# Kernel optimization log

Hardware: AMD Instinct MI355X
Metric: run time of the kernel (lower is better)

The kernel has to match this reference:

```python
import jax, jax.numpy as jnp
import numpy as np

N = 50000      # nodes
E = 800000     # edges (avg degree 16)
F_IN = 128
H = 128        # hidden_channels
C = 10         # num_classes
S = 5          # Chebyshev order K
B = 8          # graphs in batch


def setup_inputs() -> dict:
    key = jax.random.key(0)
    ks = jax.random.split(key, 9)
    x = jax.random.normal(ks[0], (N, F_IN), jnp.float32)
    edge_index = jax.random.randint(ks[1], (2, E), 0, N, dtype=jnp.int64)
    batch = jnp.sort(jax.random.randint(ks[2], (N,), 0, B, dtype=jnp.int64))
    lambda_max = 2.0 * jnp.ones((B,), jnp.float32)
    W1 = jax.random.normal(ks[3], (S, F_IN, H), jnp.float32) * 0.05
    b1 = jax.random.normal(ks[4], (H,), jnp.float32) * 0.05
    W2 = jax.random.normal(ks[5], (S, H, H), jnp.float32) * 0.05
    b2 = jax.random.normal(ks[6], (H,), jnp.float32) * 0.05
    Wlin = jax.random.normal(ks[7], (H, C), jnp.float32) * 0.05
    blin = jax.random.normal(ks[8], (C,), jnp.float32) * 0.05
    return {"x": x, "edge_index": edge_index, "batch": batch,
            "lambda_max": lambda_max, "W1": W1, "b1": b1,
            "W2": W2, "b2": b2, "Wlin": Wlin, "blin": blin}


def _cheb_conv(x, row, col, w_edge, diag, W, b):
    # scaled Laplacian matvec: L_hat v = scatter(w_edge * v[col] -> row) + diag * v
    def Lhat(v):
        msg = v[col] * w_edge[:, None]                       # [E, d]
        return jax.ops.segment_sum(msg, row, num_segments=N) + diag[:, None] * v

    Tx0 = x
    out = Tx0 @ W[0]
    Tx1 = Lhat(Tx0)
    out = out + Tx1 @ W[1]
    for k in range(2, W.shape[0]):                           # Chebyshev recurrence
        Tx2 = 2.0 * Lhat(Tx1) - Tx0
        out = out + Tx2 @ W[k]
        Tx0, Tx1 = Tx1, Tx2
    return out + b


def reference(x, edge_index, batch, lambda_max, W1, b1, W2, b2, Wlin, blin):
    row, col = edge_index[0], edge_index[1]
    # sym-normalized Laplacian L = I - D^{-1/2} A D^{-1/2}; L_hat = 2L/lambda_max - I
    deg = jax.ops.segment_sum(jnp.ones((E,), x.dtype), row, num_segments=N)
    dis = jnp.where(deg > 0, jax.lax.rsqrt(jnp.maximum(deg, 1e-12)), 0.0)
    lam_e = lambda_max[batch[row]]                           # per-edge lambda_max
    w_edge = -2.0 * dis[row] * dis[col] / lam_e              # off-diagonal of L_hat
    diag = 2.0 / lambda_max[batch] - 1.0                     # diagonal of L_hat per node

    h = jax.nn.relu(_cheb_conv(x, row, col, w_edge, diag, W1, b1))
    h = jax.nn.relu(_cheb_conv(h, row, col, w_edge, diag, W2, b2))

    # global_mean_pool over batch assignment
    sums = jax.ops.segment_sum(h, batch, num_segments=B)     # [B, H]
    counts = jax.ops.segment_sum(jnp.ones((N, 1), h.dtype), batch, num_segments=B)
    pooled = sums / jnp.maximum(counts, 1.0)
    return pooled @ Wlin + blin                              # [B, C] logits (softmax unused in forward)
```

## Files before the change

kernel.cpp:

```cpp
#include <hip/hip_runtime.h>
#include <stdint.h>

typedef __attribute__((ext_vector_type(8))) short bf16x8;
typedef __attribute__((ext_vector_type(4))) float f32x4;

__device__ __forceinline__ float bf16lo_to_f(uint32_t u) { return __uint_as_float(u << 16); }
__device__ __forceinline__ float bf16hi_to_f(uint32_t u) { return __uint_as_float(u & 0xffff0000u); }
__device__ __forceinline__ uint16_t f_to_bf16(float f) {
    uint32_t u = __float_as_uint(f);
    uint32_t r = u + 0x7fff + ((u >> 16) & 1);
    return (uint16_t)(r >> 16);
}


#define BINCH 4096

__global__ void __launch_bounds__(256) k_bhist(const int* __restrict__ row,
                                               int* __restrict__ bhist, int E) {
    __shared__ int sh[256];
    int t = threadIdx.x;
    sh[t] = 0;
    __syncthreads();
    int stride = gridDim.x * blockDim.x;
    for (int e = blockIdx.x * blockDim.x + t; e < E; e += stride)
        atomicAdd(&sh[row[e] >> 8], 1);
    __syncthreads();
    if (sh[t]) atomicAdd(&bhist[t], sh[t]);
}

__global__ void k_bscan(const int* __restrict__ bhist, int* __restrict__ gbase,
                        int* __restrict__ gcur, float* __restrict__ mS, int nbk, int N) {
    __shared__ int sh[256];
    int t = threadIdx.x;
    int v = t < nbk ? bhist[t] : 0;
    sh[t] = v;
    __syncthreads();
    for (int o = 1; o < 256; o <<= 1) {
        int u = (t >= o) ? sh[t - o] : 0;
        __syncthreads();
        sh[t] += u;
        __syncthreads();
    }
    gbase[t] = sh[t] - v;
    gcur[t] = sh[t] - v;
    if (t == 255) gbase[256] = sh[255];
    if (t < 5) mS[(size_t)t * (N + 1) + N] = 0.f;
}

__global__ void __launch_bounds__(256) k_bin(const int* __restrict__ row,
        const int* __restrict__ col, int* __restrict__ gcur,
        uint32_t* __restrict__ bout, int E) {
    __shared__ uint32_t stage[BINCH];
    __shared__ int hist[256], hscan[256], hcur[256], gofs[256];
    int t = threadIdx.x;
    int e0 = blockIdx.x * BINCH;
    int ecnt = min(BINCH, E - e0);
    hist[t] = 0;
    __syncthreads();
    for (int i = t; i < ecnt; i += 256)
        atomicAdd(&hist[row[e0 + i] >> 8], 1);
    __syncthreads();
    int v = hist[t];
    hscan[t] = v;
    __syncthreads();
    for (int o = 1; o < 256; o <<= 1) {
        int u = (t >= o) ? hscan[t - o] : 0;
        __syncthreads();
        hscan[t] += u;
        __syncthreads();
    }
    hcur[t] = hscan[t] - v;
    __syncthreads();
    for (int i = t; i < ecnt; i += 256) {
        int r = row[e0 + i];
        int p = atomicAdd(&hcur[r >> 8], 1);
        stage[p] = (uint32_t)(r & 255) | ((uint32_t)col[e0 + i] << 8);
    }
    __syncthreads();
    if (v > 0) gofs[t] = atomicAdd(&gcur[t], v);
    __syncthreads();
    for (int i = t; i < ecnt; i += 256) {
        int lo = 0, hi = 255;
        while (lo < hi) { int mid = (lo + hi) >> 1; if (hscan[mid] > i) hi = mid; else lo = mid + 1; }
        int b = lo;
        int local = i - (hscan[b] - hist[b]);
        bout[gofs[b] + local] = stage[i];
    }
}

__global__ void __launch_bounds__(256) k_deg2(const uint32_t* __restrict__ bout,
        const int* __restrict__ gbase, int* __restrict__ deg,
        int* __restrict__ psum, int N) {
    __shared__ int cnt[256];
    __shared__ int red[256];
    int t = threadIdx.x, b = blockIdx.x;
    cnt[t] = 0;
    __syncthreads();
    int s = gbase[b], epos = gbase[b + 1];
    for (int i = s + t; i < epos; i += 256)
        atomicAdd(&cnt[bout[i] & 255], 1);
    __syncthreads();
    int n = b * 256 + t;
    int d = cnt[t];
    if (n < N) deg[n] = d;
    red[t] = (n < N) ? ((d + 7) & ~7) : 0;
    __syncthreads();
    for (int o = 128; o > 0; o >>= 1) {
        if (t < o) red[t] += red[t + o];
        __syncthreads();
    }
    if (t == 0) psum[b] = red[0];
}

__global__ void k_offs(const int* __restrict__ deg, const int* __restrict__ psum,
                       int* __restrict__ offs,
                       const int* __restrict__ batch, const float* __restrict__ lam,
                       float* __restrict__ dis, float* __restrict__ diag,
                       int N, int nb) {
    __shared__ int pre[256];
    __shared__ int sh[256];
    int t = threadIdx.x, b = blockIdx.x;
    pre[t] = (t < b) ? psum[t] : 0;
    __syncthreads();
    for (int o = 128; o > 0; o >>= 1) {
        if (t < o) pre[t] += pre[t + o];
        __syncthreads();
    }
    int base = pre[0];
    __syncthreads();
    int idx = b * 256 + t;
    int d = idx < N ? deg[idx] : 0;
    int v = (d + 7) & ~7;
    sh[t] = v;
    __syncthreads();
    for (int o = 1; o < 256; o <<= 1) {
        int u = (t >= o) ? sh[t - o] : 0;
        __syncthreads();
        sh[t] += u;
        __syncthreads();
    }
    if (idx < N) {
        offs[idx] = base + sh[t] - v;
        dis[idx] = d > 0 ? rsqrtf((float)d) : 0.f;
        diag[idx] = 2.f / lam[batch[idx]] - 1.f;
    }
    if (b == nb - 1 && t == 255) offs[N] = base + sh[255];
}

__global__ void __launch_bounds__(256) k_ew(const uint32_t* __restrict__ bout,
        const int* __restrict__ gbase, const int* __restrict__ offs,
        const float* __restrict__ dis, const float* __restrict__ diag,
        uint2* __restrict__ ew, int N) {
    __shared__ int cur[256];
    __shared__ float srw[256];
    int t = threadIdx.x, b = blockIdx.x;
    int n = b * 256 + t;
    int o0 = n < N ? offs[n] : 0;
    cur[t] = o0;
    srw[t] = (n < N) ? (-dis[n] * (diag[n] + 1.0f)) : 0.f;
    __syncthreads();
    int s = gbase[b], epos = gbase[b + 1];
    for (int i = s + t; i < epos; i += 256) {
        uint32_t v = bout[i];
        int r = (int)(v & 255u);
        int c = (int)(v >> 8);
        int p = atomicAdd(&cur[r], 1);
        float w = srw[r] * dis[c];
        ew[p] = make_uint2((uint32_t)c << 7, __float_as_uint(w));
    }
    __syncthreads();
    if (n < N) {
        int e = cur[t];
        int pe = o0 + ((e - o0 + 7) & ~7);
        uint2 pad = make_uint2((uint32_t)N << 7, 0u);
        for (int p = e; p < pe; p++) ew[p] = pad;
    }
}

__global__ void k_prepw(const float* __restrict__ W1, uint16_t* __restrict__ Wt1,
                        const float* __restrict__ W2, uint16_t* __restrict__ Wt2) {
    int i = blockIdx.x * blockDim.x + threadIdx.x;
    const float* W = W1; uint16_t* Wt = Wt1;
    if (i >= 128 * 640) { i -= 128 * 640; W = W2; Wt = Wt2; }
    int o = i / 640, kk = i % 640;
    Wt[(size_t)o * 640 + kk] = f_to_bf16(W[(size_t)kk * 128 + o]);
}

__global__ void __launch_bounds__(256) k_castx(const float* __restrict__ x,
        uint16_t* __restrict__ Txb, int8_t* __restrict__ Txq,
        float* __restrict__ mS, int N) {
    int n = (blockIdx.x * blockDim.x + threadIdx.x) >> 6;
    int lane = threadIdx.x & 63;
    if (n >= N) return;
    float2 v = ((const float2*)x)[(size_t)n * 64 + lane];
    uint32_t p = (uint32_t)f_to_bf16(v.x) | ((uint32_t)f_to_bf16(v.y) << 16);
    ((uint32_t*)Txb)[(size_t)n * 64 + lane] = p;
    float m = fmaxf(fabsf(v.x), fabsf(v.y));
    for (int o = 1; o < 64; o <<= 1) m = fmaxf(m, __shfl_xor(m, o));
    float inv = m > 0.f ? 127.f / m : 0.f;
    int qx = (int)rintf(v.x * inv), qy = (int)rintf(v.y * inv);
    *(uint16_t*)(Txq + (size_t)n * 128 + 2 * lane) = (uint16_t)((qx & 0xff) | ((qy & 0xff) << 8));
    if (lane == 0) mS[n] = m > 0.f ? m * (1.f / 127.f) : 0.f;
}

__global__ void __launch_bounds__(256) k_lhat(
        int8_t* __restrict__ Txq, uint16_t* __restrict__ Txb,
        float* __restrict__ mS,
        const int* __restrict__ offs, const uint2* __restrict__ ew,
        const float* __restrict__ diag, int N,
        int src, int dst, int prev, float alpha, int use_prev) {
    int n = (blockIdx.x * blockDim.x + threadIdx.x) >> 6;
    int lane = threadIdx.x & 63;
    if (n >= N) return;
    int beg = offs[n], end = offs[n + 1];
    int h = lane >> 5, g = lane & 31;
    size_t sq = (size_t)(N + 1) * 128;
    const int8_t* srcq = Txq + (size_t)src * sq;
    const float* msrc = mS + (size_t)src * (N + 1);
    uint32_t lo4 = (uint32_t)g * 4;
    const uint2* ewh = ew + h;
    float a0 = 0.f, a1 = 0.f, a2 = 0.f, a3 = 0.f;
    if (beg < end) {
        uint2 ep[4];
#pragma unroll
        for (int p = 0; p < 4; p++) ep[p] = ewh[beg + 2 * p];
        int e = beg;
        while (true) {
            uint32_t q[4]; float mm[4], wv[4];
#pragma unroll
            for (int p = 0; p < 4; p++) {
                uint32_t co = ep[p].x;
                wv[p] = __uint_as_float(ep[p].y);
                q[p] = *(const uint32_t*)(srcq + co + lo4);
                mm[p] = *(const float*)((const char*)msrc + (co >> 5));
            }
            int e2 = e + 8;
            bool more = e2 < end;
            uint2 epn[4];
            if (more) {
#pragma unroll
                for (int p = 0; p < 4; p++) epn[p] = ewh[e2 + 2 * p];
            }
#pragma unroll
            for (int p = 0; p < 4; p++) {
                float f = wv[p] * mm[p];
                a0 = fmaf(f, (float)(int)(int8_t)(q[p] & 0xff), a0);
                a1 = fmaf(f, (float)(int)(int8_t)((q[p] >> 8) & 0xff), a1);
                a2 = fmaf(f, (float)(int)(int8_t)((q[p] >> 16) & 0xff), a2);
                a3 = fmaf(f, (float)(int)(int8_t)(q[p] >> 24), a3);
            }
            if (!more) break;
            e = e2;
#pragma unroll
            for (int p = 0; p < 4; p++) ep[p] = epn[p];
        }
    }
    a0 += __shfl_xor(a0, 32);
    a1 += __shfl_xor(a1, 32);
    a2 += __shfl_xor(a2, 32);
    a3 += __shfl_xor(a3, 32);
    uint32_t rq = (uint32_t)n * 128 + lo4;
    uint32_t qs = *(const uint32_t*)(srcq + rq);
    float ssc = msrc[n] * diag[n];
    a0 = fmaf(ssc, (float)(int)(int8_t)(qs & 0xff), a0);
    a1 = fmaf(ssc, (float)(int)(int8_t)((qs >> 8) & 0xff), a1);
    a2 = fmaf(ssc, (float)(int)(int8_t)((qs >> 16) & 0xff), a2);
    a3 = fmaf(ssc, (float)(int)(int8_t)(qs >> 24), a3);
    float f0 = alpha * a0, f1 = alpha * a1, f2 = alpha * a2, f3 = alpha * a3;
    if (use_prev) {
        uint32_t qp = *(const uint32_t*)(Txq + (size_t)prev * sq + rq);
        float sp = mS[(size_t)prev * (N + 1) + n];
        f0 = fmaf(-sp, (float)(int)(int8_t)(qp & 0xff), f0);
        f1 = fmaf(-sp, (float)(int)(int8_t)((qp >> 8) & 0xff), f1);
        f2 = fmaf(-sp, (float)(int)(int8_t)((qp >> 16) & 0xff), f2);
        f3 = fmaf(-sp, (float)(int)(int8_t)(qp >> 24), f3);
    }
    if (h == 0) {
        uint2 pk;
        pk.x = (uint32_t)f_to_bf16(f0) | ((uint32_t)f_to_bf16(f1) << 16);
        pk.y = (uint32_t)f_to_bf16(f2) | ((uint32_t)f_to_bf16(f3) << 16);
        *(uint2*)(Txb + (size_t)dst * (size_t)(N + 1) * 128 + (size_t)n * 128 + g * 4) = pk;
    }
    float m = fmaxf(fmaxf(fabsf(f0), fabsf(f1)), fmaxf(fabsf(f2), fabsf(f3)));
#pragma unroll
    for (int o = 1; o < 32; o <<= 1) m = fmaxf(m, __shfl_xor(m, o));
    float inv = m > 0.f ? 127.f / m : 0.f;
    if (h == 0) {
        int q0 = (int)rintf(f0 * inv), q1 = (int)rintf(f1 * inv);
        int q2 = (int)rintf(f2 * inv), q3 = (int)rintf(f3 * inv);
        uint32_t pkq = (uint32_t)(q0 & 0xff) | ((uint32_t)(q1 & 0xff) << 8) |
                       ((uint32_t)(q2 & 0xff) << 16) | ((uint32_t)(q3 & 0xff) << 24);
        *(uint32_t*)(Txq + (size_t)dst * sq + rq) = pkq;
    }
    if (lane == 0) mS[(size_t)dst * (N + 1) + n] = m * (1.f / 127.f);
}

#define BM 128
#define BK 64
#define LDT 72
#define LDC 132

__global__ void __launch_bounds__(256) k_gemm(
        const uint16_t* __restrict__ A, size_t sstride,
        const uint16_t* __restrict__ Bt,
        const float* __restrict__ bias,
        uint16_t* __restrict__ out2b,
        int8_t* __restrict__ out2q,
        float* __restrict__ msOut,
        float* __restrict__ pooled,
        const int* __restrict__ batch,
        int M, int Kdim) {
    __shared__ uint16_t smem[BM * LDT + 128 * LDT];
    uint16_t* As = smem;
    uint16_t* Bs = smem + BM * LDT;
    uint16_t* Ct = smem;
    int t = threadIdx.x;
    int w = t >> 6, lane = t & 63;
    int row0 = blockIdx.x * BM;
    int mrow = (w >> 1) * 64, ncol = (w & 1) * 64;

    int ar[4], akc[4];
#pragma unroll
    for (int rep = 0; rep < 4; rep++) {
        int d = rep * 256 + t;
        ar[rep] = d >> 3; akc[rep] = d & 7;
    }

    f32x4 acc[4][4];
#pragma unroll
    for (int i = 0; i < 4; i++)
#pragma unroll
        for (int j = 0; j < 4; j++) acc[i][j] = (f32x4){0.f, 0.f, 0.f, 0.f};

    bf16x8 pa[4], pb[4];
#pragma unroll
    for (int rep = 0; rep < 4; rep++) {
        int grow = row0 + ar[rep];
        int kk = akc[rep] * 8;
        bf16x8 va = {0, 0, 0, 0, 0, 0, 0, 0};
        if (grow < M)
            va = *(const bf16x8*)(A + (size_t)(kk >> 7) * sstride + (size_t)grow * 128 + (kk & 127));
        pa[rep] = va;
        pb[rep] = *(const bf16x8*)(Bt + (size_t)ar[rep] * Kdim + kk);
    }

    for (int k0 = 0; k0 < Kdim; k0 += BK) {
#pragma unroll
        for (int rep = 0; rep < 4; rep++) {
            *(bf16x8*)(&As[ar[rep] * LDT + akc[rep] * 8]) = pa[rep];
            *(bf16x8*)(&Bs[ar[rep] * LDT + akc[rep] * 8]) = pb[rep];
        }
        __syncthreads();
        int kn = k0 + BK;
        if (kn < Kdim) {
#pragma unroll
            for (int rep = 0; rep < 4; rep++) {
                int grow = row0 + ar[rep];
                int kk = kn + akc[rep] * 8;
                bf16x8 va = {0, 0, 0, 0, 0, 0, 0, 0};
                if (grow < M)
                    va = *(const bf16x8*)(A + (size_t)(kk >> 7) * sstride + (size_t)grow * 128 + (kk & 127));
                pa[rep] = va;
                pb[rep] = *(const bf16x8*)(Bt + (size_t)ar[rep] * Kdim + kk);
            }
        }
#pragma unroll
        for (int ks = 0; ks < BK; ks += 32) {
            bf16x8 af[4], bfr[4];
#pragma unroll
            for (int i = 0; i < 4; i++) {
                int r = mrow + i * 16 + (lane & 15);
                af[i] = *(const bf16x8*)(&As[r * LDT + ks + (lane >> 4) * 8]);
            }
#pragma unroll
            for (int j = 0; j < 4; j++) {
                int c = ncol + j * 16 + (lane & 15);
                bfr[j] = *(const bf16x8*)(&Bs[c * LDT + ks + (lane >> 4) * 8]);
            }
#pragma unroll
            for (int i = 0; i < 4; i++)
#pragma unroll
                for (int j = 0; j < 4; j++)
                    acc[i][j] = __builtin_amdgcn_mfma_f32_16x16x32_bf16(af[i], bfr[j], acc[i][j], 0, 0, 0);
        }
        __syncthreads();
    }

#pragma unroll
    for (int j = 0; j < 4; j++) {
        int c = ncol + j * 16 + (lane & 15);
        float bv = bias[c];
#pragma unroll
        for (int i = 0; i < 4; i++) {
            int rloc = mrow + i * 16 + (lane >> 4) * 4;
#pragma unroll
            for (int r = 0; r < 4; r++) {
                float v = acc[i][j][r] + bv;
                v = v > 0.f ? v : 0.f;
                Ct[(rloc + r) * LDC + c] = f_to_bf16(v);
            }
        }
    }
    __syncthreads();

    if (out2b) {
#pragma unroll
        for (int rep = 0; rep < 8; rep++) {
            int d = rep * 256 + t;
            int r = d >> 4, c8 = (d & 15) * 8;
            int grow = row0 + r;
            if (grow < M) {
                bf16x8 v = *(const bf16x8*)(&Ct[r * LDC + c8]);
                *(bf16x8*)(out2b + (size_t)grow * 128 + c8) = v;
            }
        }
    }
    if (out2q) {
        int r = t >> 1, half = t & 1;
        int grow = row0 + r;
        float vmax = 0.f;
        for (int j = 0; j < 32; j++) {
            uint32_t u = *(const uint32_t*)(&Ct[r * LDC + half * 64 + j * 2]);
            vmax = fmaxf(vmax, fmaxf(fabsf(bf16lo_to_f(u)), fabsf(bf16hi_to_f(u))));
        }
        vmax = fmaxf(vmax, __shfl_xor(vmax, 1));
        if (grow < M) {
            float inv = vmax > 0.f ? 127.f / vmax : 0.f;
            for (int j0 = 0; j0 < 16; j0++) {
                uint32_t u0 = *(const uint32_t*)(&Ct[r * LDC + half * 64 + j0 * 4]);
                uint32_t u1 = *(const uint32_t*)(&Ct[r * LDC + half * 64 + j0 * 4 + 2]);
                int q0 = (int)rintf(bf16lo_to_f(u0) * inv);
                int q1 = (int)rintf(bf16hi_to_f(u0) * inv);
                int q2 = (int)rintf(bf16lo_to_f(u1) * inv);
                int q3 = (int)rintf(bf16hi_to_f(u1) * inv);
                uint32_t pk = (uint32_t)(q0 & 0xff) | ((uint32_t)(q1 & 0xff) << 8) |
                              ((uint32_t)(q2 & 0xff) << 16) | ((uint32_t)(q3 & 0xff) << 24);
                *(uint32_t*)(out2q + (size_t)grow * 128 + half * 64 + j0 * 4) = pk;
            }
            if (half == 0) msOut[grow] = vmax * (1.f / 127.f);
        }
    }
    if (pooled) {
        int f = t & 127, r0 = (t >> 7) * 64;
        float accp = 0.f;
        int curb = -1;
        for (int r = r0; r < r0 + 64; ++r) {
            int grow = row0 + r;
            if (grow >= M) break;
            int b = batch[grow];
            if (b != curb) {
                if (curb >= 0) atomicAdd(&pooled[curb * 128 + f], accp);
                accp = 0.f; curb = b;
            }
            accp += __uint_as_float(((uint32_t)Ct[r * LDC + f]) << 16);
        }
        if (curb >= 0) atomicAdd(&pooled[curb * 128 + f], accp);
    }
}

__global__ void k_final(const float* __restrict__ pooled, const int* __restrict__ batch,
                        const float* __restrict__ Wlin, const float* __restrict__ blin,
                        float* __restrict__ out, int N, int B_, int C_) {
    __shared__ int cnt[64];
    int t = threadIdx.x;
    if (t < B_) {
        auto lb = [&](int v) {
            int lo = 0, hi = N;
            while (lo < hi) {
                int mid = (lo + hi) >> 1;
                if (batch[mid] < v) lo = mid + 1; else hi = mid;
            }
            return lo;
        };
        cnt[t] = lb(t + 1) - lb(t);
    }
    __syncthreads();
    if (t < B_ * C_) {
        int b = t / C_, c = t % C_;
        float inv = 1.f / fmaxf((float)cnt[b], 1.f);
        float acc = blin[c];
        for (int f = 0; f < 128; ++f) acc += pooled[b * 128 + f] * inv * Wlin[f * C_ + c];
        out[t] = acc;
    }
}

extern "C" void kernel_launch(void* const* d_in, const int* in_sizes, int n_in,
                              void* d_out, int out_size, void* d_ws, size_t ws_size,
                              hipStream_t stream) {
    const float* x    = (const float*)d_in[0];
    const int*   edge = (const int*)d_in[1];
    const int*   batch= (const int*)d_in[2];
    const float* lam  = (const float*)d_in[3];
    const float* W1   = (const float*)d_in[4];
    const float* b1   = (const float*)d_in[5];
    const float* W2   = (const float*)d_in[6];
    const float* b2   = (const float*)d_in[7];
    const float* Wlin = (const float*)d_in[8];
    const float* blin = (const float*)d_in[9];
    const int E  = in_sizes[1] / 2;
    const int N  = in_sizes[2];
    const int B_ = in_sizes[3];
    const int* row = edge;
    const int* col = edge + E;

    char* ws = (char*)d_ws;
    size_t off = 0;
    auto take = [&](size_t bytes) -> char* {
        char* p = ws + off;
        off = (off + bytes + 255) & ~(size_t)255;
        return p;
    };
    uint16_t* Txb    = (uint16_t*)take((size_t)5 * (N + 1) * 128 * 2);
    int8_t*   Txq    = (int8_t*)take((size_t)5 * (N + 1) * 128);
    uint2*    ew     = (uint2*)take(((size_t)E + 8 * (size_t)N) * 8);
    float*    mS     = (float*)take((size_t)5 * (N + 1) * 4);
    int*      deg    = (int*)take((size_t)N * 4);
    int*      offs   = (int*)take((size_t)(N + 1) * 4);
    float*    dis    = (float*)take((size_t)N * 4);
    float*    diag   = (float*)take((size_t)N * 4);
    uint16_t* Wt1    = (uint16_t*)take((size_t)128 * 640 * 2);
    uint16_t* Wt2    = (uint16_t*)take((size_t)128 * 640 * 2);
    float*    pooled = (float*)take((size_t)B_ * 128 * 4);
    int*      bhist  = (int*)take(257 * 4);
    int*      gbase  = (int*)take(257 * 4);
    int*      gcur   = (int*)take(257 * 4);
    const int nb = (N + 255) / 256;
    int*      psum   = (int*)take((size_t)nb * 4);
    uint32_t* bout   = (uint32_t*)((char*)Txb + (size_t)4 * (N + 1) * 256);

    hipMemsetAsync(pooled, 0, (size_t)B_ * 128 * 4 + 257 * 4, stream);

    k_bhist<<<112, 256, 0, stream>>>(row, bhist, E);
    k_bscan<<<1, 256, 0, stream>>>(bhist, gbase, gcur, mS, nb, N);
    k_bin<<<(E + BINCH - 1) / BINCH, 256, 0, stream>>>(row, col, gcur, bout, E);
    k_deg2<<<nb, 256, 0, stream>>>(bout, gbase, deg, psum, N);
    k_offs<<<nb, 256, 0, stream>>>(deg, psum, offs, batch, lam, dis, diag, N, nb);
    k_ew<<<nb, 256, 0, stream>>>(bout, gbase, offs, dis, diag, ew, N);
    k_prepw<<<(2 * 128 * 640) / 256, 256, 0, stream>>>(W1, Wt1, W2, Wt2);
    k_castx<<<(N + 3) / 4, 256, 0, stream>>>(x, Txb, Txq, mS, N);

    const int lblocks = (N + 3) / 4;
    const int gblocks = (N + BM - 1) / BM;
    const size_t ss = (size_t)(N + 1) * 128;

    k_lhat<<<lblocks, 256, 0, stream>>>(Txq, Txb, mS, offs, ew, diag, N, 0, 1, 0, 1.f, 0);
    k_lhat<<<lblocks, 256, 0, stream>>>(Txq, Txb, mS, offs, ew, diag, N, 1, 2, 0, 2.f, 1);
    k_lhat<<<lblocks, 256, 0, stream>>>(Txq, Txb, mS, offs, ew, diag, N, 2, 3, 1, 2.f, 1);
    k_lhat<<<lblocks, 256, 0, stream>>>(Txq, Txb, mS, offs, ew, diag, N, 3, 4, 2, 2.f, 1);
    k_gemm<<<gblocks, 256, 0, stream>>>(Txb, ss, Wt1, b1,
                                        Txb , Txq , mS ,
                                        (float*)nullptr, batch, N, 640);

    k_lhat<<<lblocks, 256, 0, stream>>>(Txq, Txb, mS, offs, ew, diag, N, 0, 1, 0, 1.f, 0);
    k_lhat<<<lblocks, 256, 0, stream>>>(Txq, Txb, mS, offs, ew, diag, N, 1, 2, 0, 2.f, 1);
    k_lhat<<<lblocks, 256, 0, stream>>>(Txq, Txb, mS, offs, ew, diag, N, 2, 3, 1, 2.f, 1);
    k_lhat<<<lblocks, 256, 0, stream>>>(Txq, Txb, mS, offs, ew, diag, N, 3, 4, 2, 2.f, 1);
    k_gemm<<<gblocks, 256, 0, stream>>>(Txb, ss, Wt2, b2,
                                        (uint16_t*)nullptr, (int8_t*)nullptr, (float*)nullptr,
                                        pooled, batch, N, 640);

    k_final<<<1, 128, 0, stream>>>(pooled, batch, Wlin, blin, (float*)d_out, N, B_, 10);
}
```

Measured before the change: 469.3 us.

## Merge preprocessing and Chebyshev recurrence launches into cooperative persistent kernels

Replaces the eight preprocessing kernels with one cooperative kernel that runs the phases separated by grid.sync(). It also replaces the four per-layer L_hat launches with one persistent cooperative kernel that loops over nodes and prefetches the next node's offsets. The goal is to cut kernel launch overhead and tail idle time between the many short dependent launches. In exchange, the persistent grid is capped by occupancy, which may lower parallelism for latency hiding in the gather phase. The old multi-launch path remains as a fallback if the cooperative launch fails.

```diff
diff --git a/kernel.cpp b/kernel.cpp
--- a/kernel.cpp
+++ b/kernel.cpp
@@ -1,5 +1,8 @@
 #include <hip/hip_runtime.h>
+#include <hip/hip_cooperative_groups.h>
 #include <stdint.h>
+
+namespace cg = cooperative_groups;
 
 typedef __attribute__((ext_vector_type(8))) short bf16x8;
 typedef __attribute__((ext_vector_type(4))) float f32x4;
@@ -203,16 +206,203 @@
     if (lane == 0) mS[n] = m > 0.f ? m * (1.f / 127.f) : 0.f;
 }
 
-__global__ void __launch_bounds__(256) k_lhat(
+__global__ void __launch_bounds__(256) k_pre(
+        const float* __restrict__ x,
+        const int* __restrict__ row, const int* __restrict__ col,
+        const int* __restrict__ batch, const float* __restrict__ lam,
+        const float* __restrict__ W1, uint16_t* __restrict__ Wt1,
+        const float* __restrict__ W2, uint16_t* __restrict__ Wt2,
+        int* __restrict__ bhist, int* __restrict__ gbase, int* __restrict__ gcur,
+        uint32_t* __restrict__ bout, int* __restrict__ deg, int* __restrict__ psum,
+        int* __restrict__ offs, float* __restrict__ dis, float* __restrict__ diag,
+        uint2* __restrict__ ew, float* __restrict__ mS,
+        uint16_t* __restrict__ Txb, int8_t* __restrict__ Txq,
+        int E, int N, int nb, int nchunks) {
+    __shared__ uint32_t shb[5120];
+    cg::grid_group grid = cg::this_grid();
+    int t = threadIdx.x, b = blockIdx.x;
+    int gstride = gridDim.x * 256;
+
+    {
+        int* sh = (int*)shb;
+        sh[t] = 0;
+        __syncthreads();
+        for (int e = b * 256 + t; e < E; e += gstride)
+            atomicAdd(&sh[row[e] >> 8], 1);
+        __syncthreads();
+        if (sh[t]) atomicAdd(&bhist[t], sh[t]);
+    }
+    for (int i = b * 256 + t; i < 2 * 128 * 640; i += gstride) {
+        int ii = i;
+        const float* W = W1; uint16_t* Wt = Wt1;
+        if (ii >= 128 * 640) { ii -= 128 * 640; W = W2; Wt = Wt2; }
+        int o = ii / 640, kk = ii % 640;
+        Wt[(size_t)o * 640 + kk] = f_to_bf16(W[(size_t)kk * 128 + o]);
+    }
+    {
+        int lane = t & 63;
+        int gw = b * 4 + (t >> 6);
+        int tw = gridDim.x * 4;
+        for (int n = gw; n < N; n += tw) {
+            float2 v = ((const float2*)x)[(size_t)n * 64 + lane];
+            uint32_t p = (uint32_t)f_to_bf16(v.x) | ((uint32_t)f_to_bf16(v.y) << 16);
+            ((uint32_t*)Txb)[(size_t)n * 64 + lane] = p;
+            float m = fmaxf(fabsf(v.x), fabsf(v.y));
+            for (int o = 1; o < 64; o <<= 1) m = fmaxf(m, __shfl_xor(m, o));
+            float inv = m > 0.f ? 127.f / m : 0.f;
+            int qx = (int)rintf(v.x * inv), qy = (int)rintf(v.y * inv);
+            *(uint16_t*)(Txq + (size_t)n * 128 + 2 * lane) =
+                (uint16_t)((qx & 0xff) | ((qy & 0xff) << 8));
+            if (lane == 0) mS[n] = m > 0.f ? m * (1.f / 127.f) : 0.f;
+        }
+    }
+    grid.sync();
+
+    if (b == 0) {
+        int* sh = (int*)shb;
+        int v = bhist[t];
+        sh[t] = v;
+        __syncthreads();
+        for (int o = 1; o < 256; o <<= 1) {
+            int u = (t >= o) ? sh[t - o] : 0;
+            __syncthreads();
+            sh[t] += u;
+            __syncthreads();
+        }
+        gbase[t] = sh[t] - v;
+        gcur[t] = sh[t] - v;
+        if (t == 255) gbase[256] = sh[255];
+        if (t < 5) mS[(size_t)t * (N + 1) + N] = 0.f;
+    }
+    grid.sync();
+
+    if (b < nchunks) {
+        uint32_t* stage = shb;
+        int* hist  = (int*)(shb + 4096);
+        int* hscan = (int*)(shb + 4352);
+        int* hcur  = (int*)(shb + 4608);
+        int* gofs  = (int*)(shb + 4864);
+        int e0 = b * BINCH;
+        int ecnt = min(BINCH, E - e0);
+        hist[t] = 0;
+        __syncthreads();
+        for (int i = t; i < ecnt; i += 256)
+            atomicAdd(&hist[row[e0 + i] >> 8], 1);
+        __syncthreads();
+        int v = hist[t];
+        hscan[t] = v;
+        __syncthreads();
+        for (int o = 1; o < 256; o <<= 1) {
+            int u = (t >= o) ? hscan[t - o] : 0;
+            __syncthreads();
+            hscan[t] += u;
+            __syncthreads();
+        }
+        hcur[t] = hscan[t] - v;
+        __syncthreads();
+        for (int i = t; i < ecnt; i += 256) {
+            int r = row[e0 + i];
+            int p = atomicAdd(&hcur[r >> 8], 1);
+            stage[p] = (uint32_t)(r & 255) | ((uint32_t)col[e0 + i] << 8);
+        }
+        __syncthreads();
+        if (v > 0) gofs[t] = atomicAdd(&gcur[t], v);
+        __syncthreads();
+        for (int i = t; i < ecnt; i += 256) {
+            int lo = 0, hi = 255;
+            while (lo < hi) { int mid = (lo + hi) >> 1; if (hscan[mid] > i) hi = mid; else lo = mid + 1; }
+            int bb = lo;
+            int local = i - (hscan[bb] - hist[bb]);
+            bout[gofs[bb] + local] = stage[i];
+        }
+    }
+    grid.sync();
+
+    if (b < nb) {
+        int* cnt = (int*)shb;
+        int* red = (int*)(shb + 256);
+        cnt[t] = 0;
+        __syncthreads();
+        int s = gbase[b], epos = gbase[b + 1];
+        for (int i = s + t; i < epos; i += 256)
+            atomicAdd(&cnt[bout[i] & 255], 1);
+        __syncthreads();
+        int n = b * 256 + t;
+        int d = cnt[t];
+        if (n < N) deg[n] = d;
+        red[t] = (n < N) ? ((d + 7) & ~7) : 0;
+        __syncthreads();
+        for (int o = 128; o > 0; o >>= 1) {
+            if (t < o) red[t] += red[t + o];
+            __syncthreads();
+        }
+        if (t == 0) psum[b] = red[0];
+    }
+    grid.sync();
+
+    if (b < nb) {
+        int* pre = (int*)shb;
+        int* sh2 = (int*)(shb + 256);
+        pre[t] = (t < b) ? psum[t] : 0;
+        __syncthreads();
+        for (int o = 128; o > 0; o >>= 1) {
+            if (t < o) pre[t] += pre[t + o];
+            __syncthreads();
+        }
+        int base = pre[0];
+        __syncthreads();
+        int idx = b * 256 + t;
+        int d = idx < N ? deg[idx] : 0;
+        int v = (d + 7) & ~7;
+        sh2[t] = v;
+        __syncthreads();
+        for (int o = 1; o < 256; o <<= 1) {
+            int u = (t >= o) ? sh2[t - o] : 0;
+            __syncthreads();
+            sh2[t] += u;
+            __syncthreads();
+        }
+        if (idx < N) {
+            offs[idx] = base + sh2[t] - v;
+            dis[idx] = d > 0 ? rsqrtf((float)d) : 0.f;
+            diag[idx] = 2.f / lam[batch[idx]] - 1.f;
+        }
+        if (b == nb - 1 && t == 255) offs[N] = base + sh2[255];
+    }
+    grid.sync();
+
+    if (b < nb) {
+        int* cur = (int*)shb;
+        float* srw = (float*)(shb + 256);
+        int n = b * 256 + t;
+        int o0 = n < N ? offs[n] : 0;
+        cur[t] = o0;
+        srw[t] = (n < N) ? (-dis[n] * (diag[n] + 1.0f)) : 0.f;
+        __syncthreads();
+        int s = gbase[b], epos = gbase[b + 1];
+        for (int i = s + t; i < epos; i += 256) {
+            uint32_t v = bout[i];
+            int r = (int)(v & 255u);
+            int c = (int)(v >> 8);
+            int p = atomicAdd(&cur[r], 1);
+            float w = srw[r] * dis[c];
+            ew[p] = make_uint2((uint32_t)c << 7, __float_as_uint(w));
+        }
+        __syncthreads();
+        if (n < N) {
+            int e = cur[t];
+            int pe = o0 + ((e - o0 + 7) & ~7);
+            uint2 pad = make_uint2((uint32_t)N << 7, 0u);
+            for (int p = e; p < pe; p++) ew[p] = pad;
+        }
+    }
+}
+
+__device__ __forceinline__ void lhat_node(int n, int lane,
         int8_t* __restrict__ Txq, uint16_t* __restrict__ Txb,
-        float* __restrict__ mS,
-        const int* __restrict__ offs, const uint2* __restrict__ ew,
-        const float* __restrict__ diag, int N,
-        int src, int dst, int prev, float alpha, int use_prev) {
-    int n = (blockIdx.x * blockDim.x + threadIdx.x) >> 6;
-    int lane = threadIdx.x & 63;
-    if (n >= N) return;
-    int beg = offs[n], end = offs[n + 1];
+        float* __restrict__ mS, const uint2* __restrict__ ew, int N,
+        int beg, int end, float dgn,
+        int src, int dst, int prev, float alpha, bool use_prev) {
     int h = lane >> 5, g = lane & 31;
     size_t sq = (size_t)(N + 1) * 128;
     const int8_t* srcq = Txq + (size_t)src * sq;
@@ -261,7 +451,7 @@
     a3 += __shfl_xor(a3, 32);
     uint32_t rq = (uint32_t)n * 128 + lo4;
     uint32_t qs = *(const uint32_t*)(srcq + rq);
-    float ssc = msrc[n] * diag[n];
+    float ssc = msrc[n] * dgn;
     a0 = fmaf(ssc, (float)(int)(int8_t)(qs & 0xff), a0);
     a1 = fmaf(ssc, (float)(int)(int8_t)((qs >> 8) & 0xff), a1);
     a2 = fmaf(ssc, (float)(int)(int8_t)((qs >> 16) & 0xff), a2);
@@ -293,6 +483,53 @@
         *(uint32_t*)(Txq + (size_t)dst * sq + rq) = pkq;
     }
     if (lane == 0) mS[(size_t)dst * (N + 1) + n] = m * (1.f / 127.f);
+}
+
+__global__ void __launch_bounds__(256) k_lhat(
+        int8_t* __restrict__ Txq, uint16_t* __restrict__ Txb,
+        float* __restrict__ mS,
+        const int* __restrict__ offs, const uint2* __restrict__ ew,
+        const float* __restrict__ diag, int N,
+        int src, int dst, int prev, float alpha, int use_prev) {
+    int n = (blockIdx.x * blockDim.x + threadIdx.x) >> 6;
+    int lane = threadIdx.x & 63;
+    if (n >= N) return;
+    lhat_node(n, lane, Txq, Txb, mS, ew, N, offs[n], offs[n + 1], diag[n],
+              src, dst, prev, alpha, use_prev != 0);
+}
+
+__global__ void __launch_bounds__(256, 4) k_layer(
+        int8_t* __restrict__ Txq, uint16_t* __restrict__ Txb,
+        float* __restrict__ mS,
+        const int* __restrict__ offs, const uint2* __restrict__ ew,
+        const float* __restrict__ diag, int N) {
+    cg::grid_group grid = cg::this_grid();
+    int lane = threadIdx.x & 63;
+    int gw = blockIdx.x * 4 + (threadIdx.x >> 6);
+    int tw = gridDim.x * 4;
+
+#define LHAT_PHASE(SRC, DST, PRV, ALPHA, UP)                                   \
+    {                                                                          \
+        int n = gw, pb = 0, pe = 0; float pd = 0.f;                            \
+        if (n < N) { pb = offs[n]; pe = offs[n + 1]; pd = diag[n]; }           \
+        while (n < N) {                                                        \
+            int beg = pb, ee = pe; float dg = pd;                              \
+            int n2 = n + tw;                                                   \
+            if (n2 < N) { pb = offs[n2]; pe = offs[n2 + 1]; pd = diag[n2]; }   \
+            lhat_node(n, lane, Txq, Txb, mS, ew, N, beg, ee, dg,               \
+                      SRC, DST, PRV, ALPHA, UP);                               \
+            n = n2;                                                            \
+        }                                                                      \
+    }
+
+    LHAT_PHASE(0, 1, 0, 1.f, false);
+    grid.sync();
+    LHAT_PHASE(1, 2, 0, 2.f, true);
+    grid.sync();
+    LHAT_PHASE(2, 3, 1, 2.f, true);
+    grid.sync();
+    LHAT_PHASE(3, 4, 2, 2.f, true);
+#undef LHAT_PHASE
 }
 
 #define BM 128
@@ -530,31 +767,78 @@
 
     hipMemsetAsync(pooled, 0, (size_t)B_ * 128 * 4 + 257 * 4, stream);
 
-    k_bhist<<<112, 256, 0, stream>>>(row, bhist, E);
-    k_bscan<<<1, 256, 0, stream>>>(bhist, gbase, gcur, mS, nb, N);
-    k_bin<<<(E + BINCH - 1) / BINCH, 256, 0, stream>>>(row, col, gcur, bout, E);
-    k_deg2<<<nb, 256, 0, stream>>>(bout, gbase, deg, psum, N);
-    k_offs<<<nb, 256, 0, stream>>>(deg, psum, offs, batch, lam, dis, diag, N, nb);
-    k_ew<<<nb, 256, 0, stream>>>(bout, gbase, offs, dis, diag, ew, N);
-    k_prepw<<<(2 * 128 * 640) / 256, 256, 0, stream>>>(W1, Wt1, W2, Wt2);
-    k_castx<<<(N + 3) / 4, 256, 0, stream>>>(x, Txb, Txq, mS, N);
-
+    const int nchunks = (E + BINCH - 1) / BINCH;
+    const int PREB = nchunks > nb ? nchunks : nb;
     const int lblocks = (N + 3) / 4;
     const int gblocks = (N + BM - 1) / BM;
     const size_t ss = (size_t)(N + 1) * 128;
 
-    k_lhat<<<lblocks, 256, 0, stream>>>(Txq, Txb, mS, offs, ew, diag, N, 0, 1, 0, 1.f, 0);
-    k_lhat<<<lblocks, 256, 0, stream>>>(Txq, Txb, mS, offs, ew, diag, N, 1, 2, 0, 2.f, 1);
-    k_lhat<<<lblocks, 256, 0, stream>>>(Txq, Txb, mS, offs, ew, diag, N, 2, 3, 1, 2.f, 1);
-    k_lhat<<<lblocks, 256, 0, stream>>>(Txq, Txb, mS, offs, ew, diag, N, 3, 4, 2, 2.f, 1);
+    static int s_layerGrid = 0;
+    static int s_preMax = 0;
+    if (s_layerGrid == 0) {
+        int perCU = 0;
+        if (hipOccupancyMaxActiveBlocksPerMultiprocessor(&perCU, k_layer, 256, 0) != hipSuccess
+            || perCU <= 0) perCU = 2;
+        int g = perCU * 256;
+        if (g > 2048) g = 2048;
+        s_layerGrid = g;
+        int perCUp = 0;
+        if (hipOccupancyMaxActiveBlocksPerMultiprocessor(&perCUp, k_pre, 256, 0) != hipSuccess
+            || perCUp <= 0) perCUp = 1;
+        s_preMax = perCUp * 256;
+    }
+
+    bool preCoop = (PREB <= s_preMax);
+    if (preCoop) {
+        int E_ = E, N_ = N, nb_ = nb, nc_ = nchunks;
+        const float* x_ = x; const int* row_ = row; const int* col_ = col;
+        const int* batch_ = batch; const float* lam_ = lam;
+        const float* W1_ = W1; const float* W2_ = W2;
+        void* args[] = {
+            (void*)&x_, (void*)&row_, (void*)&col_, (void*)&batch_, (void*)&lam_,
+            (void*)&W1_, (void*)&Wt1, (void*)&W2_, (void*)&Wt2,
+            (void*)&bhist, (void*)&gbase, (void*)&gcur,
+            (void*)&bout, (void*)&deg, (void*)&psum,
+            (void*)&offs, (void*)&dis, (void*)&diag,
+            (void*)&ew, (void*)&mS, (void*)&Txb, (void*)&Txq,
+            (void*)&E_, (void*)&N_, (void*)&nb_, (void*)&nc_ };
+        hipError_t e = hipLaunchCooperativeKernel((void*)k_pre, dim3(PREB), dim3(256),
+                                                  args, 0, stream);
+        if (e != hipSuccess) { (void)hipGetLastError(); preCoop = false; }
+    }
+    if (!preCoop) {
+        k_bhist<<<112, 256, 0, stream>>>(row, bhist, E);
+        k_bscan<<<1, 256, 0, stream>>>(bhist, gbase, gcur, mS, nb, N);
+        k_bin<<<nchunks, 256, 0, stream>>>(row, col, gcur, bout, E);
+        k_deg2<<<nb, 256, 0, stream>>>(bout, gbase, deg, psum, N);
+        k_offs<<<nb, 256, 0, stream>>>(deg, psum, offs, batch, lam, dis, diag, N, nb);
+        k_ew<<<nb, 256, 0, stream>>>(bout, gbase, offs, dis, diag, ew, N);
+        k_prepw<<<(2 * 128 * 640) / 256, 256, 0, stream>>>(W1, Wt1, W2, Wt2);
+        k_castx<<<(N + 3) / 4, 256, 0, stream>>>(x, Txb, Txq, mS, N);
+    }
+
+    auto run_layer = [&]() {
+        int N_ = N;
+        int8_t* Txq_ = Txq; uint16_t* Txb_ = Txb; float* mS_ = mS;
+        const int* offs_ = offs; const uint2* ew_ = ew; const float* diag_ = diag;
+        void* largs[] = { (void*)&Txq_, (void*)&Txb_, (void*)&mS_,
+                          (void*)&offs_, (void*)&ew_, (void*)&diag_, (void*)&N_ };
+        hipError_t e = hipLaunchCooperativeKernel((void*)k_layer, dim3(s_layerGrid),
+                                                  dim3(256), largs, 0, stream);
+        if (e != hipSuccess) {
+            (void)hipGetLastError();
+            k_lhat<<<lblocks, 256, 0, stream>>>(Txq, Txb, mS, offs, ew, diag, N, 0, 1, 0, 1.f, 0);
+            k_lhat<<<lblocks, 256, 0, stream>>>(Txq, Txb, mS, offs, ew, diag, N, 1, 2, 0, 2.f, 1);
+            k_lhat<<<lblocks, 256, 0, stream>>>(Txq, Txb, mS, offs, ew, diag, N, 2, 3, 1, 2.f, 1);
+            k_lhat<<<lblocks, 256, 0, stream>>>(Txq, Txb, mS, offs, ew, diag, N, 3, 4, 2, 2.f, 1);
+        }
+    };
+
+    run_layer();
     k_gemm<<<gblocks, 256, 0, stream>>>(Txb, ss, Wt1, b1,
-                                        Txb , Txq , mS ,
+                                        Txb, Txq, mS,
                                         (float*)nullptr, batch, N, 640);
-
-    k_lhat<<<lblocks, 256, 0, stream>>>(Txq, Txb, mS, offs, ew, diag, N, 0, 1, 0, 1.f, 0);
-    k_lhat<<<lblocks, 256, 0, stream>>>(Txq, Txb, mS, offs, ew, diag, N, 1, 2, 0, 2.f, 1);
-    k_lhat<<<lblocks, 256, 0, stream>>>(Txq, Txb, mS, offs, ew, diag, N, 2, 3, 1, 2.f, 1);
-    k_lhat<<<lblocks, 256, 0, stream>>>(Txq, Txb, mS, offs, ew, diag, N, 3, 4, 2, 2.f, 1);
+    run_layer();
     k_gemm<<<gblocks, 256, 0, stream>>>(Txb, ss, Wt2, b2,
                                         (uint16_t*)nullptr, (int8_t*)nullptr, (float*)nullptr,
                                         pooled, batch, N, 640);
```

Result: slower. 1.241 ms (+164.4%).

## Process two nodes per wavefront in Laplacian SpMV and fuse preprocessing kernels

Applied to the files above, without the earlier changes.

The Lhat gather kernel now handles two nodes per 64-lane wave, interleaving their edge loops so more independent gathers are in flight per wave. Node begin/end offsets and the diagonal are packed into one 16-byte record, read with a single load instead of separate offs and diag reads. The histogram, weight transpose and x cast/quantize kernels are merged into one grid-stride launch to cut launch count. In exchange there are more registers per thread and lane divergence when the two nodes have different degrees.

```diff
diff --git a/kernel.cpp b/kernel.cpp
--- a/kernel.cpp
+++ b/kernel.cpp
@@ -15,17 +15,46 @@
 
 #define BINCH 4096
 
-__global__ void __launch_bounds__(256) k_bhist(const int* __restrict__ row,
-                                               int* __restrict__ bhist, int E) {
+__global__ void __launch_bounds__(256) k_pre1(
+        const int* __restrict__ row, int* __restrict__ bhist,
+        const float* __restrict__ W1, uint16_t* __restrict__ Wt1,
+        const float* __restrict__ W2, uint16_t* __restrict__ Wt2,
+        const float* __restrict__ x, uint16_t* __restrict__ Txb,
+        int8_t* __restrict__ Txq, float* __restrict__ mS,
+        int E, int N) {
     __shared__ int sh[256];
-    int t = threadIdx.x;
+    int t = threadIdx.x, b = blockIdx.x;
+    int gstride = gridDim.x * 256;
     sh[t] = 0;
     __syncthreads();
-    int stride = gridDim.x * blockDim.x;
-    for (int e = blockIdx.x * blockDim.x + t; e < E; e += stride)
+    for (int e = b * 256 + t; e < E; e += gstride)
         atomicAdd(&sh[row[e] >> 8], 1);
     __syncthreads();
     if (sh[t]) atomicAdd(&bhist[t], sh[t]);
+    for (int i = b * 256 + t; i < 2 * 128 * 640; i += gstride) {
+        int ii = i;
+        const float* W = W1; uint16_t* Wt = Wt1;
+        if (ii >= 128 * 640) { ii -= 128 * 640; W = W2; Wt = Wt2; }
+        int o = ii / 640, kk = ii % 640;
+        Wt[(size_t)o * 640 + kk] = f_to_bf16(W[(size_t)kk * 128 + o]);
+    }
+    {
+        int lane = t & 63;
+        int gw = b * 4 + (t >> 6);
+        int tw = gridDim.x * 4;
+        for (int n = gw; n < N; n += tw) {
+            float2 v = ((const float2*)x)[(size_t)n * 64 + lane];
+            uint32_t p = (uint32_t)f_to_bf16(v.x) | ((uint32_t)f_to_bf16(v.y) << 16);
+            ((uint32_t*)Txb)[(size_t)n * 64 + lane] = p;
+            float m = fmaxf(fabsf(v.x), fabsf(v.y));
+            for (int o = 1; o < 64; o <<= 1) m = fmaxf(m, __shfl_xor(m, o));
+            float inv = m > 0.f ? 127.f / m : 0.f;
+            int qx = (int)rintf(v.x * inv), qy = (int)rintf(v.y * inv);
+            *(uint16_t*)(Txq + (size_t)n * 128 + 2 * lane) =
+                (uint16_t)((qx & 0xff) | ((qy & 0xff) << 8));
+            if (lane == 0) mS[n] = m > 0.f ? m * (1.f / 127.f) : 0.f;
+        }
+    }
 }
 
 __global__ void k_bscan(const int* __restrict__ bhist, int* __restrict__ gbase,
@@ -116,6 +145,7 @@
                        int* __restrict__ offs,
                        const int* __restrict__ batch, const float* __restrict__ lam,
                        float* __restrict__ dis, float* __restrict__ diag,
+                       uint4* __restrict__ nh,
                        int N, int nb) {
     __shared__ int pre[256];
     __shared__ int sh[256];
@@ -140,9 +170,13 @@
         __syncthreads();
     }
     if (idx < N) {
-        offs[idx] = base + sh[t] - v;
+        int beg = base + sh[t] - v;
+        float dgv = 2.f / lam[batch[idx]] - 1.f;
+        offs[idx] = beg;
         dis[idx] = d > 0 ? rsqrtf((float)d) : 0.f;
-        diag[idx] = 2.f / lam[batch[idx]] - 1.f;
+        diag[idx] = dgv;
+        nh[idx] = make_uint4((uint32_t)beg, (uint32_t)(base + sh[t]),
+                             __float_as_uint(dgv), 0u);
     }
     if (b == nb - 1 && t == 255) offs[N] = base + sh[255];
 }
@@ -177,122 +211,151 @@
     }
 }
 
-__global__ void k_prepw(const float* __restrict__ W1, uint16_t* __restrict__ Wt1,
-                        const float* __restrict__ W2, uint16_t* __restrict__ Wt2) {
-    int i = blockIdx.x * blockDim.x + threadIdx.x;
-    const float* W = W1; uint16_t* Wt = Wt1;
-    if (i >= 128 * 640) { i -= 128 * 640; W = W2; Wt = Wt2; }
-    int o = i / 640, kk = i % 640;
-    Wt[(size_t)o * 640 + kk] = f_to_bf16(W[(size_t)kk * 128 + o]);
-}
-
-__global__ void __launch_bounds__(256) k_castx(const float* __restrict__ x,
-        uint16_t* __restrict__ Txb, int8_t* __restrict__ Txq,
-        float* __restrict__ mS, int N) {
-    int n = (blockIdx.x * blockDim.x + threadIdx.x) >> 6;
-    int lane = threadIdx.x & 63;
-    if (n >= N) return;
-    float2 v = ((const float2*)x)[(size_t)n * 64 + lane];
-    uint32_t p = (uint32_t)f_to_bf16(v.x) | ((uint32_t)f_to_bf16(v.y) << 16);
-    ((uint32_t*)Txb)[(size_t)n * 64 + lane] = p;
-    float m = fmaxf(fabsf(v.x), fabsf(v.y));
-    for (int o = 1; o < 64; o <<= 1) m = fmaxf(m, __shfl_xor(m, o));
-    float inv = m > 0.f ? 127.f / m : 0.f;
-    int qx = (int)rintf(v.x * inv), qy = (int)rintf(v.y * inv);
-    *(uint16_t*)(Txq + (size_t)n * 128 + 2 * lane) = (uint16_t)((qx & 0xff) | ((qy & 0xff) << 8));
-    if (lane == 0) mS[n] = m > 0.f ? m * (1.f / 127.f) : 0.f;
-}
-
-__global__ void __launch_bounds__(256) k_lhat(
+__global__ void __launch_bounds__(256) k_lhat2(
         int8_t* __restrict__ Txq, uint16_t* __restrict__ Txb,
         float* __restrict__ mS,
-        const int* __restrict__ offs, const uint2* __restrict__ ew,
-        const float* __restrict__ diag, int N,
+        const uint4* __restrict__ nh, const uint2* __restrict__ ew,
+        int N,
         int src, int dst, int prev, float alpha, int use_prev) {
-    int n = (blockIdx.x * blockDim.x + threadIdx.x) >> 6;
+    int wid = (blockIdx.x * blockDim.x + threadIdx.x) >> 6;
     int lane = threadIdx.x & 63;
-    if (n >= N) return;
-    int beg = offs[n], end = offs[n + 1];
+    int n0 = wid * 2;
+    if (n0 >= N) return;
+    int n1 = n0 + 1;
+    bool has1 = n1 < N;
     int h = lane >> 5, g = lane & 31;
     size_t sq = (size_t)(N + 1) * 128;
     const int8_t* srcq = Txq + (size_t)src * sq;
     const float* msrc = mS + (size_t)src * (N + 1);
     uint32_t lo4 = (uint32_t)g * 4;
     const uint2* ewh = ew + h;
-    float a0 = 0.f, a1 = 0.f, a2 = 0.f, a3 = 0.f;
-    if (beg < end) {
-        uint2 ep[4];
-#pragma unroll
-        for (int p = 0; p < 4; p++) ep[p] = ewh[beg + 2 * p];
-        int e = beg;
-        while (true) {
-            uint32_t q[4]; float mm[4], wv[4];
+
+    uint4 h0 = nh[n0];
+    uint4 h1 = has1 ? nh[n1] : make_uint4(0, 0, 0, 0);
+    int e0 = (int)h0.x, end0 = (int)h0.y;
+    int e1 = (int)h1.x, end1 = (int)h1.y;
+    float dg0 = __uint_as_float(h0.z), dg1 = __uint_as_float(h1.z);
+
+    float A00 = 0.f, A01 = 0.f, A02 = 0.f, A03 = 0.f;
+    float A10 = 0.f, A11 = 0.f, A12 = 0.f, A13 = 0.f;
+
+    bool a0 = e0 < end0, a1 = e1 < end1;
+    uint2 p0[4], p1[4];
+    if (a0) {
+#pragma unroll
+        for (int p = 0; p < 4; p++) p0[p] = ewh[e0 + 2 * p];
+    }
+    if (a1) {
+#pragma unroll
+        for (int p = 0; p < 4; p++) p1[p] = ewh[e1 + 2 * p];
+    }
+    while (a0 | a1) {
+        uint32_t q0[4], q1[4];
+        float m0[4], w0[4], m1[4], w1[4];
+        if (a0) {
 #pragma unroll
             for (int p = 0; p < 4; p++) {
-                uint32_t co = ep[p].x;
-                wv[p] = __uint_as_float(ep[p].y);
-                q[p] = *(const uint32_t*)(srcq + co + lo4);
-                mm[p] = *(const float*)((const char*)msrc + (co >> 5));
-            }
-            int e2 = e + 8;
-            bool more = e2 < end;
-            uint2 epn[4];
-            if (more) {
-#pragma unroll
-                for (int p = 0; p < 4; p++) epn[p] = ewh[e2 + 2 * p];
-            }
+                uint32_t co = p0[p].x;
+                w0[p] = __uint_as_float(p0[p].y);
+                q0[p] = *(const uint32_t*)(srcq + co + lo4);
+                m0[p] = *(const float*)((const char*)msrc + (co >> 5));
+            }
+        }
+        if (a1) {
 #pragma unroll
             for (int p = 0; p < 4; p++) {
-                float f = wv[p] * mm[p];
-                a0 = fmaf(f, (float)(int)(int8_t)(q[p] & 0xff), a0);
-                a1 = fmaf(f, (float)(int)(int8_t)((q[p] >> 8) & 0xff), a1);
-                a2 = fmaf(f, (float)(int)(int8_t)((q[p] >> 16) & 0xff), a2);
-                a3 = fmaf(f, (float)(int)(int8_t)(q[p] >> 24), a3);
-            }
-            if (!more) break;
-            e = e2;
-#pragma unroll
-            for (int p = 0; p < 4; p++) ep[p] = epn[p];
-        }
-    }
-    a0 += __shfl_xor(a0, 32);
-    a1 += __shfl_xor(a1, 32);
-    a2 += __shfl_xor(a2, 32);
-    a3 += __shfl_xor(a3, 32);
-    uint32_t rq = (uint32_t)n * 128 + lo4;
-    uint32_t qs = *(const uint32_t*)(srcq + rq);
-    float ssc = msrc[n] * diag[n];
-    a0 = fmaf(ssc, (float)(int)(int8_t)(qs & 0xff), a0);
-    a1 = fmaf(ssc, (float)(int)(int8_t)((qs >> 8) & 0xff), a1);
-    a2 = fmaf(ssc, (float)(int)(int8_t)((qs >> 16) & 0xff), a2);
-    a3 = fmaf(ssc, (float)(int)(int8_t)(qs >> 24), a3);
-    float f0 = alpha * a0, f1 = alpha * a1, f2 = alpha * a2, f3 = alpha * a3;
-    if (use_prev) {
-        uint32_t qp = *(const uint32_t*)(Txq + (size_t)prev * sq + rq);
-        float sp = mS[(size_t)prev * (N + 1) + n];
-        f0 = fmaf(-sp, (float)(int)(int8_t)(qp & 0xff), f0);
-        f1 = fmaf(-sp, (float)(int)(int8_t)((qp >> 8) & 0xff), f1);
-        f2 = fmaf(-sp, (float)(int)(int8_t)((qp >> 16) & 0xff), f2);
-        f3 = fmaf(-sp, (float)(int)(int8_t)(qp >> 24), f3);
-    }
-    if (h == 0) {
-        uint2 pk;
-        pk.x = (uint32_t)f_to_bf16(f0) | ((uint32_t)f_to_bf16(f1) << 16);
-        pk.y = (uint32_t)f_to_bf16(f2) | ((uint32_t)f_to_bf16(f3) << 16);
-        *(uint2*)(Txb + (size_t)dst * (size_t)(N + 1) * 128 + (size_t)n * 128 + g * 4) = pk;
-    }
-    float m = fmaxf(fmaxf(fabsf(f0), fabsf(f1)), fmaxf(fabsf(f2), fabsf(f3)));
-#pragma unroll
-    for (int o = 1; o < 32; o <<= 1) m = fmaxf(m, __shfl_xor(m, o));
-    float inv = m > 0.f ? 127.f / m : 0.f;
-    if (h == 0) {
-        int q0 = (int)rintf(f0 * inv), q1 = (int)rintf(f1 * inv);
-        int q2 = (int)rintf(f2 * inv), q3 = (int)rintf(f3 * inv);
-        uint32_t pkq = (uint32_t)(q0 & 0xff) | ((uint32_t)(q1 & 0xff) << 8) |
-                       ((uint32_t)(q2 & 0xff) << 16) | ((uint32_t)(q3 & 0xff) << 24);
-        *(uint32_t*)(Txq + (size_t)dst * sq + rq) = pkq;
-    }
-    if (lane == 0) mS[(size_t)dst * (N + 1) + n] = m * (1.f / 127.f);
+                uint32_t co = p1[p].x;
+                w1[p] = __uint_as_float(p1[p].y);
+                q1[p] = *(const uint32_t*)(srcq + co + lo4);
+                m1[p] = *(const float*)((const char*)msrc + (co >> 5));
+            }
+        }
+        int e0n = e0 + 8, e1n = e1 + 8;
+        bool a0n = a0 && (e0n < end0);
+        bool a1n = a1 && (e1n < end1);
+        uint2 p0n[4], p1n[4];
+        if (a0n) {
+#pragma unroll
+            for (int p = 0; p < 4; p++) p0n[p] = ewh[e0n + 2 * p];
+        }
+        if (a1n) {
+#pragma unroll
+            for (int p = 0; p < 4; p++) p1n[p] = ewh[e1n + 2 * p];
+        }
+        if (a0) {
+#pragma unroll
+            for (int p = 0; p < 4; p++) {
+                float f = w0[p] * m0[p];
+                A00 = fmaf(f, (float)(int)(int8_t)(q0[p] & 0xff), A00);
+                A01 = fmaf(f, (float)(int)(int8_t)((q0[p] >> 8) & 0xff), A01);
+                A02 = fmaf(f, (float)(int)(int8_t)((q0[p] >> 16) & 0xff), A02);
+                A03 = fmaf(f, (float)(int)(int8_t)(q0[p] >> 24), A03);
+            }
+        }
+        if (a1) {
+#pragma unroll
+            for (int p = 0; p < 4; p++) {
+                float f = w1[p] * m1[p];
+                A10 = fmaf(f, (float)(int)(int8_t)(q1[p] & 0xff), A10);
+                A11 = fmaf(f, (float)(int)(int8_t)((q1[p] >> 8) & 0xff), A11);
+                A12 = fmaf(f, (float)(int)(int8_t)((q1[p] >> 16) & 0xff), A12);
+                A13 = fmaf(f, (float)(int)(int8_t)(q1[p] >> 24), A13);
+            }
+        }
+        e0 = e0n; e1 = e1n;
+        if (a0n) {
+#pragma unroll
+            for (int p = 0; p < 4; p++) p0[p] = p0n[p];
+        }
+        if (a1n) {
+#pragma unroll
+            for (int p = 0; p < 4; p++) p1[p] = p1n[p];
+        }
+        a0 = a0n; a1 = a1n;
+    }
+
+    auto epi = [&](int n, float f0a, float f1a, float f2a, float f3a, float dgn) {
+        float b0 = f0a + __shfl_xor(f0a, 32);
+        float b1 = f1a + __shfl_xor(f1a, 32);
+        float b2 = f2a + __shfl_xor(f2a, 32);
+        float b3 = f3a + __shfl_xor(f3a, 32);
+        uint32_t rq = (uint32_t)n * 128 + lo4;
+        uint32_t qs = *(const uint32_t*)(srcq + rq);
+        float ssc = msrc[n] * dgn;
+        b0 = fmaf(ssc, (float)(int)(int8_t)(qs & 0xff), b0);
+        b1 = fmaf(ssc, (float)(int)(int8_t)((qs >> 8) & 0xff), b1);
+        b2 = fmaf(ssc, (float)(int)(int8_t)((qs >> 16) & 0xff), b2);
+        b3 = fmaf(ssc, (float)(int)(int8_t)(qs >> 24), b3);
+        float f0 = alpha * b0, f1 = alpha * b1, f2 = alpha * b2, f3 = alpha * b3;
+        if (use_prev) {
+            uint32_t qp = *(const uint32_t*)(Txq + (size_t)prev * sq + rq);
+            float sp = mS[(size_t)prev * (N + 1) + n];
+            f0 = fmaf(-sp, (float)(int)(int8_t)(qp & 0xff), f0);
+            f1 = fmaf(-sp, (float)(int)(int8_t)((qp >> 8) & 0xff), f1);
+            f2 = fmaf(-sp, (float)(int)(int8_t)((qp >> 16) & 0xff), f2);
+            f3 = fmaf(-sp, (float)(int)(int8_t)(qp >> 24), f3);
+        }
+        if (h == 0) {
+            uint2 pk;
+            pk.x = (uint32_t)f_to_bf16(f0) | ((uint32_t)f_to_bf16(f1) << 16);
+            pk.y = (uint32_t)f_to_bf16(f2) | ((uint32_t)f_to_bf16(f3) << 16);
+            *(uint2*)(Txb + (size_t)dst * (size_t)(N + 1) * 128 + (size_t)n * 128 + g * 4) = pk;
+        }
+        float m = fmaxf(fmaxf(fabsf(f0), fabsf(f1)), fmaxf(fabsf(f2), fabsf(f3)));
+#pragma unroll
+        for (int o = 1; o < 32; o <<= 1) m = fmaxf(m, __shfl_xor(m, o));
+        float inv = m > 0.f ? 127.f / m : 0.f;
+        if (h == 0) {
+            int q0v = (int)rintf(f0 * inv), q1v = (int)rintf(f1 * inv);
+            int q2v = (int)rintf(f2 * inv), q3v = (int)rintf(f3 * inv);
+            uint32_t pkq = (uint32_t)(q0v & 0xff) | ((uint32_t)(q1v & 0xff) << 8) |
+                           ((uint32_t)(q2v & 0xff) << 16) | ((uint32_t)(q3v & 0xff) << 24);
+            *(uint32_t*)(Txq + (size_t)dst * sq + rq) = pkq;
+        }
+        if (lane == 0) mS[(size_t)dst * (N + 1) + n] = m * (1.f / 127.f);
+    };
+    epi(n0, A00, A01, A02, A03, dg0);
+    if (has1) epi(n1, A10, A11, A12, A13, dg1);
 }
 
 #define BM 128
@@ -518,6 +581,7 @@
     int*      offs   = (int*)take((size_t)(N + 1) * 4);
     float*    dis    = (float*)take((size_t)N * 4);
     float*    diag   = (float*)take((size_t)N * 4);
+    uint4*    nh     = (uint4*)take((size_t)N * 16);
     uint16_t* Wt1    = (uint16_t*)take((size_t)128 * 640 * 2);
     uint16_t* Wt2    = (uint16_t*)take((size_t)128 * 640 * 2);
     float*    pooled = (float*)take((size_t)B_ * 128 * 4);
@@ -530,31 +594,31 @@
 
     hipMemsetAsync(pooled, 0, (size_t)B_ * 128 * 4 + 257 * 4, stream);
 
-    k_bhist<<<112, 256, 0, stream>>>(row, bhist, E);
+    const int nchunks = (E + BINCH - 1) / BINCH;
+
+    k_pre1<<<1024, 256, 0, stream>>>(row, bhist, W1, Wt1, W2, Wt2,
+                                     x, Txb, Txq, mS, E, N);
     k_bscan<<<1, 256, 0, stream>>>(bhist, gbase, gcur, mS, nb, N);
-    k_bin<<<(E + BINCH - 1) / BINCH, 256, 0, stream>>>(row, col, gcur, bout, E);
+    k_bin<<<nchunks, 256, 0, stream>>>(row, col, gcur, bout, E);
     k_deg2<<<nb, 256, 0, stream>>>(bout, gbase, deg, psum, N);
-    k_offs<<<nb, 256, 0, stream>>>(deg, psum, offs, batch, lam, dis, diag, N, nb);
+    k_offs<<<nb, 256, 0, stream>>>(deg, psum, offs, batch, lam, dis, diag, nh, N, nb);
     k_ew<<<nb, 256, 0, stream>>>(bout, gbase, offs, dis, diag, ew, N);
-    k_prepw<<<(2 * 128 * 640) / 256, 256, 0, stream>>>(W1, Wt1, W2, Wt2);
-    k_castx<<<(N + 3) / 4, 256, 0, stream>>>(x, Txb, Txq, mS, N);
-
-    const int lblocks = (N + 3) / 4;
+
+    const int l2blocks = (N + 7) / 8;
     const int gblocks = (N + BM - 1) / BM;
     const size_t ss = (size_t)(N + 1) * 128;
 
-    k_lhat<<<lblocks, 256, 0, stream>>>(Txq, Txb, mS, offs, ew, diag, N, 0, 1, 0, 1.f, 0);
-    k_lhat<<<lblocks, 256, 0, stream>>>(Txq, Txb, mS, offs, ew, diag, N, 1, 2, 0, 2.f, 1);
-    k_lhat<<<lblocks, 256, 0, stream>>>(Txq, Txb, mS, offs, ew, diag, N, 2, 3, 1, 2.f, 1);
-    k_lhat<<<lblocks, 256, 0, stream>>>(Txq, Txb, mS, offs, ew, diag, N, 3, 4, 2, 2.f, 1);
+    k_lhat2<<<l2blocks, 256, 0, stream>>>(Txq, Txb, mS, nh, ew, N, 0, 1, 0, 1.f, 0);
+    k_lhat2<<<l2blocks, 256, 0, stream>>>(Txq, Txb, mS, nh, ew, N, 1, 2, 0, 2.f, 1);
+    k_lhat2<<<l2blocks, 256, 0, stream>>>(Txq, Txb, mS, nh, ew, N, 2, 3, 1, 2.f, 1);
+    k_lhat2<<<l2blocks, 256, 0, stream>>>(Txq, Txb, mS, nh, ew, N, 3, 4, 2, 2.f, 1);
     k_gemm<<<gblocks, 256, 0, stream>>>(Txb, ss, Wt1, b1,
-                                        Txb , Txq , mS ,
+                                        Txb, Txq, mS,
                                         (float*)nullptr, batch, N, 640);
-
-    k_lhat<<<lblocks, 256, 0, stream>>>(Txq, Txb, mS, offs, ew, diag, N, 0, 1, 0, 1.f, 0);
-    k_lhat<<<lblocks, 256, 0, stream>>>(Txq, Txb, mS, offs, ew, diag, N, 1, 2, 0, 2.f, 1);
-    k_lhat<<<lblocks, 256, 0, stream>>>(Txq, Txb, mS, offs, ew, diag, N, 2, 3, 1, 2.f, 1);
-    k_lhat<<<lblocks, 256, 0, stream>>>(Txq, Txb, mS, offs, ew, diag, N, 3, 4, 2, 2.f, 1);
+    k_lhat2<<<l2blocks, 256, 0, stream>>>(Txq, Txb, mS, nh, ew, N, 0, 1, 0, 1.f, 0);
+    k_lhat2<<<l2blocks, 256, 0, stream>>>(Txq, Txb, mS, nh, ew, N, 1, 2, 0, 2.f, 1);
+    k_lhat2<<<l2blocks, 256, 0, stream>>>(Txq, Txb, mS, nh, ew, N, 2, 3, 1, 2.f, 1);
+    k_lhat2<<<l2blocks, 256, 0, stream>>>(Txq, Txb, mS, nh, ew, N, 3, 4, 2, 2.f, 1);
     k_gemm<<<gblocks, 256, 0, stream>>>(Txb, ss, Wt2, b2,
                                         (uint16_t*)nullptr, (int8_t*)nullptr, (float*)nullptr,
                                         pooled, batch, N, 640);
```

Measured after the change: 602.8 us. 28.5% more time.
